# Kernel optimization log

Measured on AMD Instinct MI355X. Metric: run time of the kernel, lower is better.

Reference implementation:

```python
import jax, jax.numpy as jnp
import numpy as np

B, T, C, H, W = 16, 5, 512, 16, 16
NUM_FEAT = 10
K_IN = T * H * W          # 1280, conv1/G3 in_channels
G_OUT = NUM_FEAT * H * W  # 2560, G3 out_channels


def setup_inputs() -> dict:
    key = jax.random.key(0)
    ks = jax.random.split(key, 9)
    inp = {
        "input": jax.random.normal(ks[0], (B, T, C, H, W), dtype=jnp.float32),
        "input1": jax.random.normal(ks[1], (B, T, C, H, W), dtype=jnp.float32),
        "act_weights": jax.random.uniform(ks[2], (3,), dtype=jnp.float32),
        # Conv1d kernels with kernel_size=1 stored as [out_ch, in_ch]
        "conv1_w": jax.random.normal(ks[3], (NUM_FEAT, K_IN), dtype=jnp.float32) / np.sqrt(K_IN),
        "conv1_b": jax.random.normal(ks[4], (NUM_FEAT,), dtype=jnp.float32) * 0.01,
        "G3_w": jax.random.normal(ks[5], (G_OUT, K_IN), dtype=jnp.float32) / np.sqrt(K_IN),
        "G3_b": jax.random.normal(ks[6], (G_OUT,), dtype=jnp.float32) * 0.01,
        "ffnn1_w": jax.random.normal(ks[7], (C, C), dtype=jnp.float32) / np.sqrt(C),
        "ffnn1_b": jax.random.normal(ks[8], (C,), dtype=jnp.float32) * 0.01,
    }
    return inp


def reference(input, input1, act_weights, conv1_w, conv1_b, G3_w, G3_b, ffnn1_w, ffnn1_b):
    b, t, c, h, w = input.shape
    nf = conv1_w.shape[0]
    # [B,T,C,H,W] -> [B,C,T*H*W] -> transpose to [B, T*H*W, C] (conv1d channel axis = T*H*W)
    x = jnp.transpose(input, (0, 2, 1, 3, 4)).reshape(b, c, t * h * w)
    x = jnp.swapaxes(x, 1, 2)  # [B, K_IN, C]

    # conv1 (1x1 conv == GEMM over channel axis): [B, nf, C]
    c1 = jnp.einsum("fk,bkc->bfc", conv1_w, x) + conv1_b[None, :, None]
    # transpose -> [B, C, nf]; AvgPool1d(nf) -> mean over nf -> [B, C]
    pooled = jnp.mean(jnp.swapaxes(c1, 1, 2), axis=-1)
    # shared linear (same ffnn1 used in all three branches)
    pre = pooled @ ffnn1_w.T + ffnn1_b  # [B, C]

    # G3: [B, G_OUT, C] -> permute -> [B, C, G_OUT]
    g3 = jnp.einsum("gk,bkc->bgc", G3_w, x) + G3_b[None, :, None]
    g3 = jnp.swapaxes(g3, 1, 2)  # [B, C, G_OUT]

    # diag_embed(v) @ M == v[..., None] * M  -> fuse the three branches into one scale
    scale = (act_weights[0] * jax.nn.relu(pre)
             + act_weights[1] * jax.nn.sigmoid(pre)
             + act_weights[2] * jax.nn.softmax(pre, axis=1))  # [B, C]

    out = scale[:, :, None] * g3  # [B, C, nf*H*W]
    out = out.reshape(b, c, nf, h, w)
    return jnp.transpose(out, (0, 2, 1, 3, 4))  # [B, nf, C, H, W]
```

## Files before the change

kernel.cpp:

```cpp
#include <hip/hip_runtime.h>
#include <hip/hip_bf16.h>
#include <stdint.h>

#define B_   16
#define T_   5
#define C_   512
#define HW_  256
#define NF_  10
#define KIN_ 1280
#define GOUT_ 2560

typedef __attribute__((ext_vector_type(8))) short s16x8;
typedef __attribute__((ext_vector_type(4))) float f32x4;
typedef unsigned short u16;

__device__ __forceinline__ u16 f2bf(float x) {
    unsigned int u = __float_as_uint(x);
    return (u16)((u + 0x7FFFu + ((u >> 16) & 1u)) >> 16);
}

#define CASTW_N8  (GOUT_ * KIN_ / 8)
#define CASTW_BLKS (CASTW_N8 / 256)

__global__ __launch_bounds__(256) void k_init(const float* __restrict__ conv1_w,
                        const float* __restrict__ conv1_b,
                        float* __restrict__ wbar, float* __restrict__ bbar,
                        const float* __restrict__ g3w,
                        u16* __restrict__ wsA) {
    if (blockIdx.x < 5) {
        int k = blockIdx.x * 256 + threadIdx.x;
        float s = 0.f;
        #pragma unroll
        for (int f = 0; f < NF_; ++f) s += conv1_w[f * KIN_ + k];
        wbar[k] = s * (1.0f / NF_);
        if (blockIdx.x == 0 && threadIdx.x == 0) {
            float sb = 0.f;
            #pragma unroll
            for (int f = 0; f < NF_; ++f) sb += conv1_b[f];
            *bbar = sb * (1.0f / NF_);
        }
        return;
    }
    int i = (blockIdx.x - 5) * 256 + threadIdx.x;
    if (i < CASTW_N8) {
        const float4* s = reinterpret_cast<const float4*>(g3w) + (size_t)i * 2;
        float4 v0 = s[0], v1 = s[1];
        union { u16 h[8]; int4 v; } u;
        u.h[0] = f2bf(v0.x); u.h[1] = f2bf(v0.y); u.h[2] = f2bf(v0.z); u.h[3] = f2bf(v0.w);
        u.h[4] = f2bf(v1.x); u.h[5] = f2bf(v1.y); u.h[6] = f2bf(v1.z); u.h[7] = f2bf(v1.w);
        reinterpret_cast<int4*>(wsA)[i] = u.v;
    }
}

__global__ void k_wbar(const float* __restrict__ conv1_w,
                       const float* __restrict__ conv1_b,
                       float* __restrict__ wbar, float* __restrict__ bbar) {
    int k = blockIdx.x * blockDim.x + threadIdx.x;
    if (k < KIN_) {
        float s = 0.f;
        #pragma unroll
        for (int f = 0; f < NF_; ++f) s += conv1_w[f * KIN_ + k];
        wbar[k] = s * (1.0f / NF_);
    }
    if (blockIdx.x == 0 && threadIdx.x == 0) {
        float s = 0.f;
        #pragma unroll
        for (int f = 0; f < NF_; ++f) s += conv1_b[f];
        *bbar = s * (1.0f / NF_);
    }
}

#define FUSE_BLKS (B_ * C_)

__global__ __launch_bounds__(256) void k_prep(const float* __restrict__ in,
                         const float* __restrict__ wbar,
                         const float* __restrict__ bbar,
                         float* __restrict__ pooled,
                         u16* __restrict__ X) {
    int bc = blockIdx.x;
    int b = bc >> 9;
    int c = bc & 511;
    int tid = threadIdx.x;

    float s = 0.f;
    if (tid < 160) {
        int t   = tid >> 5;
        int hw0 = (tid & 31) * 8;
        size_t off = ((size_t)(b * T_ + t) * C_ + c) * HW_ + hw0;
        const float4* ip = reinterpret_cast<const float4*>(in + off);
        float4 v0 = ip[0], v1 = ip[1];
        const float4* wp = reinterpret_cast<const float4*>(wbar + t * HW_ + hw0);
        float4 w0 = wp[0], w1 = wp[1];
        s = v0.x * w0.x + v0.y * w0.y + v0.z * w0.z + v0.w * w0.w
          + v1.x * w1.x + v1.y * w1.y + v1.z * w1.z + v1.w * w1.w;
        union { u16 h[8]; int4 q; } u;
        u.h[0] = f2bf(v0.x); u.h[1] = f2bf(v0.y); u.h[2] = f2bf(v0.z); u.h[3] = f2bf(v0.w);
        u.h[4] = f2bf(v1.x); u.h[5] = f2bf(v1.y); u.h[6] = f2bf(v1.z); u.h[7] = f2bf(v1.w);
        reinterpret_cast<int4*>(X + off)[0] = u.q;
    }

    #pragma unroll
    for (int off = 32; off > 0; off >>= 1) s += __shfl_down(s, off, 64);
    __shared__ float red[4];
    int wid = tid >> 6, lane = tid & 63;
    if (lane == 0) red[wid] = s;
    __syncthreads();
    if (tid == 0) {
        float tot = red[0] + red[1] + red[2] + red[3];
        pooled[bc] = tot + *bbar;
    }
}

__global__ __launch_bounds__(256) void k_pooled(const float* __restrict__ in,
                         const float* __restrict__ wbar,
                         const float* __restrict__ bbar,
                         float* __restrict__ pooled) {
    int bc = blockIdx.x;
    int b = bc >> 9;
    int c = bc & 511;
    int hw = threadIdx.x;
    const float* base = in + ((size_t)(b * T_) * C_ + c) * HW_;
    float s = 0.f;
    #pragma unroll
    for (int t = 0; t < T_; ++t)
        s = fmaf(wbar[t * HW_ + hw], base[(size_t)t * C_ * HW_ + hw], s);
    #pragma unroll
    for (int off = 32; off > 0; off >>= 1) s += __shfl_down(s, off, 64);
    __shared__ float red[4];
    int wid = threadIdx.x >> 6, lane = threadIdx.x & 63;
    if (lane == 0) red[wid] = s;
    __syncthreads();
    if (threadIdx.x == 0) {
        float tot = red[0] + red[1] + red[2] + red[3];
        pooled[bc] = tot + *bbar;
    }
}

__global__ __launch_bounds__(256) void k_pre(const float* __restrict__ pooled,
                       const float* __restrict__ ffnn1_w,
                       const float* __restrict__ ffnn1_b,
                       float* __restrict__ pre) {
    int b   = blockIdx.x >> 4;
    int grp = blockIdx.x & 15;
    int wid = threadIdx.x >> 6, lane = threadIdx.x & 63;

    const float4* pp = reinterpret_cast<const float4*>(pooled + b * C_ + lane * 8);
    float4 pa = pp[0], pb = pp[1];

    #pragma unroll
    for (int rr = 0; rr < 8; ++rr) {
        int c = grp * 32 + wid * 8 + rr;
        const float4* wr = reinterpret_cast<const float4*>(ffnn1_w + (size_t)c * C_ + lane * 8);
        float4 wa = wr[0], wb2 = wr[1];
        float d = pa.x * wa.x + pa.y * wa.y + pa.z * wa.z + pa.w * wa.w
                + pb.x * wb2.x + pb.y * wb2.y + pb.z * wb2.z + pb.w * wb2.w;
        #pragma unroll
        for (int off = 32; off > 0; off >>= 1) d += __shfl_xor(d, off, 64);
        if (lane == 0) pre[b * C_ + c] = d + ffnn1_b[c];
    }
}

__global__ __launch_bounds__(512) void k_scale(const float* __restrict__ pooled,
                        const float* __restrict__ ffnn1_w,
                        const float* __restrict__ ffnn1_b,
                        const float* __restrict__ actw,
                        float* __restrict__ scale) {
    int b = blockIdx.x;
    int c = threadIdx.x;
    __shared__ float sp[C_];
    __shared__ float red[8];

    sp[c] = pooled[b * C_ + c];
    __syncthreads();

    float acc = ffnn1_b[c];
    const float* wr = ffnn1_w + (size_t)c * C_;
    #pragma unroll 8
    for (int j = 0; j < C_; ++j) acc = fmaf(wr[j], sp[j], acc);

    int wid = c >> 6, lane = c & 63;
    float m = acc;
    #pragma unroll
    for (int off = 32; off > 0; off >>= 1) m = fmaxf(m, __shfl_down(m, off, 64));
    if (lane == 0) red[wid] = m;
    __syncthreads();
    if (c == 0) {
        float mm = red[0];
        #pragma unroll
        for (int i = 1; i < 8; ++i) mm = fmaxf(mm, red[i]);
        red[0] = mm;
    }
    __syncthreads();
    m = red[0];
    __syncthreads();

    float e = __expf(acc - m);
    float s = e;
    #pragma unroll
    for (int off = 32; off > 0; off >>= 1) s += __shfl_down(s, off, 64);
    if (lane == 0) red[wid] = s;
    __syncthreads();
    if (c == 0) {
        float ss = 0.f;
        #pragma unroll
        for (int i = 0; i < 8; ++i) ss += red[i];
        red[0] = ss;
    }
    __syncthreads();
    s = red[0];

    float w0 = actw[0], w1 = actw[1], w2 = actw[2];
    float val = w0 * fmaxf(acc, 0.f)
              + w1 * (1.f / (1.f + __expf(-acc)))
              + w2 * (e / s);
    scale[b * C_ + c] = val;
}

#define BM 320
#define BN 256
#define BK 32
#define NKT (KIN_ / BK)
#define ABUF (BM * BK)
#define BBUF (BN * BK)
#define BUFU (ABUF + BBUF)

__device__ __forceinline__ void gload16(const void* g, void* l) {
    __builtin_amdgcn_global_load_lds(
        (const __attribute__((address_space(1))) void*)g,
        (__attribute__((address_space(3))) void*)l, 16, 0, 0);
}

__global__ __launch_bounds__(512, 1) void k_gemm_mfma(
    const u16* __restrict__ A,
    const u16* __restrict__ X,
    const float* __restrict__ g3b,
    const float* __restrict__ pre,
    const float* __restrict__ actw,
    float* __restrict__ out)
{
    __shared__ u16 lds[3 * BUFU];
    __shared__ float sS[BN];
    __shared__ float redm[8], reds[8];

    int orig = blockIdx.x;
    int xcd  = orig & 7;
    int idx  = orig >> 3;
    int nt   = xcd * 4 + (idx >> 3);
    int gt   = idx & 7;
    int g0   = gt * BM;
    int b    = nt >> 1;
    int c0   = (nt & 1) * BN;

    int tid = threadIdx.x;
    int lane = tid & 63, wid = tid >> 6;
    int wr = wid >> 2, wc = wid & 3;
    int lrow = lane & 15, lslot = lane >> 4;

    int offA0, offA1, offA2, offB0, offB1;
    {
        int q, r, p;
        q = tid;         r = q >> 2; p = q & 3; offA0 = r * KIN_ + (p ^ ((r >> 1) & 3)) * 8;
        q = 512 + tid;   r = q >> 2; p = q & 3; offA1 = r * KIN_ + (p ^ ((r >> 1) & 3)) * 8;
        q = 1024 + tid;  r = q >> 2; p = q & 3; offA2 = r * KIN_ + (p ^ ((r >> 1) & 3)) * 8;
        q = tid;         r = q >> 2; p = q & 3; offB0 = r * HW_  + (p ^ ((r >> 1) & 3)) * 8;
        q = 512 + tid;   r = q >> 2; p = q & 3; offB1 = r * HW_  + (p ^ ((r >> 1) & 3)) * 8;
    }
    int wb = wid * 512;

    const u16* Abase = A + (size_t)g0 * KIN_;
    #define XOFF(kt) ((((size_t)(b * T_ + ((kt) >> 3)) * C_) + c0) * HW_ + ((kt) & 7) * 32)

    #define STAGE_H1(D, sA, sX)                                              \
    {                                                                        \
        gload16((sA) + offA0, (D) + wb);                                     \
        gload16((sA) + offA1, (D) + 4096 + wb);                              \
        gload16((sX) + offB0, (D) + ABUF + wb);                              \
    }
    #define STAGE_H2(D, sA, sX)                                              \
    {                                                                        \
        if (tid < 256) gload16((sA) + offA2, (D) + 8192 + wb);               \
        gload16((sX) + offB1, (D) + ABUF + 4096 + wb);                       \
    }

    {
        float p0 = pre[b * C_ + tid];
        float aw0 = actw[0], aw1 = actw[1], aw2 = actw[2];
        float mx = p0;
        #pragma unroll
        for (int off = 32; off > 0; off >>= 1) mx = fmaxf(mx, __shfl_xor(mx, off, 64));
        if (lane == 0) redm[wid] = mx;
        __syncthreads();
        float m8 = redm[0];
        #pragma unroll
        for (int i = 1; i < 8; ++i) m8 = fmaxf(m8, redm[i]);
        float e0 = __expf(p0 - m8);
        float sm = e0;
        #pragma unroll
        for (int off = 32; off > 0; off >>= 1) sm += __shfl_xor(sm, off, 64);
        if (lane == 0) reds[wid] = sm;
        __syncthreads();
        float ssum = reds[0];
        #pragma unroll
        for (int i = 1; i < 8; ++i) ssum += reds[i];
        if ((tid >> 8) == (c0 >> 8))
            sS[tid & 255] = aw0 * fmaxf(p0, 0.f)
                          + aw1 * (1.f / (1.f + __expf(-p0)))
                          + aw2 * (e0 / ssum);
    }

    STAGE_H1(lds, Abase, X + XOFF(0));
    STAGE_H2(lds, Abase, X + XOFF(0));
    STAGE_H1(lds + BUFU, Abase + BK, X + XOFF(1));
    STAGE_H2(lds + BUFU, Abase + BK, X + XOFF(1));
    if (tid < 256) asm volatile("s_waitcnt vmcnt(5)" ::: "memory");
    else           asm volatile("s_waitcnt vmcnt(4)" ::: "memory");
    __builtin_amdgcn_s_barrier();

    f32x4 acc[10][4];
    #pragma unroll
    for (int mI = 0; mI < 10; ++mI)
        #pragma unroll
        for (int n = 0; n < 4; ++n) acc[mI][n] = (f32x4)0.f;

    int cur = 0;
    for (int t = 0; t < NKT; ++t) {
        const u16* Ac = lds + cur * BUFU;
        const u16* Bc = Ac + ABUF;
        bool pre2 = (t + 2) < NKT;
        int nx = cur + 2; if (nx >= 3) nx -= 3;
        u16* Dn = lds + nx * BUFU;
        const u16* sA = Abase + (size_t)(t + 2) * BK;
        const u16* sX = X + XOFF(pre2 ? (t + 2) : 0);

        s16x8 b0[4], a0[5];
        #pragma unroll
        for (int n = 0; n < 4; ++n) {
            int r = wc * 64 + n * 16 + lrow;
            int p = lslot ^ ((r >> 1) & 3);
            b0[n] = *reinterpret_cast<const s16x8*>(Bc + r * BK + p * 8);
        }
        #pragma unroll
        for (int mI = 0; mI < 5; ++mI) {
            int r = wr * 160 + mI * 16 + lrow;
            int p = lslot ^ ((r >> 1) & 3);
            a0[mI] = *reinterpret_cast<const s16x8*>(Ac + r * BK + p * 8);
        }
        if (pre2) STAGE_H1(Dn, sA, sX);
        __builtin_amdgcn_s_barrier();
        asm volatile("s_waitcnt lgkmcnt(0)" ::: "memory");
        __builtin_amdgcn_sched_barrier(0);
        __builtin_amdgcn_s_setprio(1);
        #pragma unroll
        for (int mI = 0; mI < 5; ++mI)
            #pragma unroll
            for (int n = 0; n < 4; ++n)
                acc[mI][n] = __builtin_amdgcn_mfma_f32_16x16x32_bf16(
                                a0[mI], b0[n], acc[mI][n], 0, 0, 0);
        __builtin_amdgcn_s_setprio(0);

        s16x8 a1[5];
        #pragma unroll
        for (int mI = 0; mI < 5; ++mI) {
            int r = wr * 160 + (mI + 5) * 16 + lrow;
            int p = lslot ^ ((r >> 1) & 3);
            a1[mI] = *reinterpret_cast<const s16x8*>(Ac + r * BK + p * 8);
        }
        if (pre2) STAGE_H2(Dn, sA, sX);
        __builtin_amdgcn_s_barrier();
        asm volatile("s_waitcnt lgkmcnt(0)" ::: "memory");
        __builtin_amdgcn_sched_barrier(0);
        __builtin_amdgcn_s_setprio(1);
        #pragma unroll
        for (int mI = 0; mI < 5; ++mI)
            #pragma unroll
            for (int n = 0; n < 4; ++n)
                acc[mI + 5][n] = __builtin_amdgcn_mfma_f32_16x16x32_bf16(
                                    a1[mI], b0[n], acc[mI + 5][n], 0, 0, 0);
        __builtin_amdgcn_s_setprio(0);

        if (pre2) {
            if (tid < 256) asm volatile("s_waitcnt vmcnt(5)" ::: "memory");
            else           asm volatile("s_waitcnt vmcnt(4)" ::: "memory");
        } else {
            asm volatile("s_waitcnt vmcnt(0)" ::: "memory");
        }
        __builtin_amdgcn_s_barrier();
        ++cur; if (cur >= 3) cur -= 3;
    }

    #pragma unroll
    for (int n = 0; n < 4; ++n) {
        int cl = wc * 64 + n * 16 + lrow;
        int c  = c0 + cl;
        float sc = sS[cl];
        #pragma unroll
        for (int mI = 0; mI < 10; ++mI) {
            int g  = g0 + wr * 160 + mI * 16 + lslot * 4;
            int f  = g >> 8;
            int hw = g & 255;
            float4 bias = *reinterpret_cast<const float4*>(g3b + g);
            f32x4 v = acc[mI][n];
            float4 o;
            o.x = sc * (v[0] + bias.x);
            o.y = sc * (v[1] + bias.y);
            o.z = sc * (v[2] + bias.z);
            o.w = sc * (v[3] + bias.w);
            *reinterpret_cast<float4*>(
                out + (((size_t)(b * NF_ + f) * C_ + c) * HW_ + hw)) = o;
        }
    }
    #undef XOFF
    #undef STAGE_H1
    #undef STAGE_H2
}

#define FBM 128
#define FBN 128
#define FBK 32
__global__ __launch_bounds__(256) void k_gemm_fp32(
    const float* __restrict__ in,
    const float* __restrict__ g3w,
    const float* __restrict__ g3b,
    const float* __restrict__ scale,
    float* __restrict__ out)
{
    int b  = blockIdx.y;
    int gt = blockIdx.x >> 2;
    int ct = blockIdx.x & 3;
    int g0 = gt * FBM, c0 = ct * FBN;
    int tid = threadIdx.x;
    int ty = tid & 15;
    int tx = tid >> 4;

    __shared__ float As[FBK][FBM + 4];
    __shared__ float Bs[FBK][FBN + 4];

    float acc[8][8];
    #pragma unroll
    for (int i = 0; i < 8; ++i)
        #pragma unroll
        for (int j = 0; j < 8; ++j) acc[i][j] = 0.f;

    for (int k0 = 0; k0 < KIN_; k0 += FBK) {
        int t   = k0 >> 8;
        int hw0 = k0 & 255;
        #pragma unroll
        for (int p = 0; p < 16; ++p) {
            int idx = tid + p * 256;
            int kk = idx & 31, gg = idx >> 5;
            As[kk][gg] = g3w[(size_t)(g0 + gg) * KIN_ + k0 + kk];
        }
        const float* bsrc = in + ((size_t)(b * T_ + t) * C_ + c0) * HW_ + hw0;
        #pragma unroll
        for (int p = 0; p < 16; ++p) {
            int idx = tid + p * 256;
            int kk = idx & 31, cc = idx >> 5;
            Bs[kk][cc] = bsrc[(size_t)cc * HW_ + kk];
        }
        __syncthreads();
        #pragma unroll
        for (int kk = 0; kk < FBK; ++kk) {
            float a[8], bb[8];
            #pragma unroll
            for (int i = 0; i < 8; ++i) a[i] = As[kk][ty * 8 + i];
            #pragma unroll
            for (int j = 0; j < 8; ++j) bb[j] = Bs[kk][tx * 8 + j];
            #pragma unroll
            for (int i = 0; i < 8; ++i)
                #pragma unroll
                for (int j = 0; j < 8; ++j)
                    acc[i][j] = fmaf(a[i], bb[j], acc[i][j]);
        }
        __syncthreads();
    }

    int gl = ty * 8;
    int g  = g0 + gl;
    int f  = g >> 8;
    int hw = g & 255;
    #pragma unroll
    for (int j = 0; j < 8; ++j) {
        int c = c0 + tx * 8 + j;
        float sc = scale[b * C_ + c];
        float* op = out + (((size_t)(b * NF_ + f) * C_ + c) * HW_ + hw);
        float4 v0, v1;
        v0.x = sc * (acc[0][j] + g3b[g + 0]);
        v0.y = sc * (acc[1][j] + g3b[g + 1]);
        v0.z = sc * (acc[2][j] + g3b[g + 2]);
        v0.w = sc * (acc[3][j] + g3b[g + 3]);
        v1.x = sc * (acc[4][j] + g3b[g + 4]);
        v1.y = sc * (acc[5][j] + g3b[g + 5]);
        v1.z = sc * (acc[6][j] + g3b[g + 6]);
        v1.w = sc * (acc[7][j] + g3b[g + 7]);
        reinterpret_cast<float4*>(op)[0] = v0;
        reinterpret_cast<float4*>(op)[1] = v1;
    }
}

extern "C" void kernel_launch(void* const* d_in, const int* in_sizes, int n_in,
                              void* d_out, int out_size, void* d_ws, size_t ws_size,
                              hipStream_t stream) {
    const float* input    = (const float*)d_in[0];
    const float* actw     = (const float*)d_in[2];
    const float* conv1_w  = (const float*)d_in[3];
    const float* conv1_b  = (const float*)d_in[4];
    const float* g3w      = (const float*)d_in[5];
    const float* g3b      = (const float*)d_in[6];
    const float* ffnn1_w  = (const float*)d_in[7];
    const float* ffnn1_b  = (const float*)d_in[8];
    float* out = (float*)d_out;

    float* ws     = (float*)d_ws;
    float* wbar   = ws;
    float* bbar   = ws + KIN_;
    float* pooled = ws + 1536;
    float* pre    = ws + 1536 + B_ * C_;
    u16* wsA = (u16*)(ws + 17920);
    u16* wsX = wsA + (size_t)GOUT_ * KIN_;
    const size_t need = 71680ull + (size_t)GOUT_ * KIN_ * 2 + (size_t)B_ * T_ * C_ * HW_ * 2;

    if (ws_size >= need) {
        k_init<<<dim3(5 + CASTW_BLKS), dim3(256), 0, stream>>>(
            conv1_w, conv1_b, wbar, bbar, g3w, wsA);
        k_prep<<<dim3(FUSE_BLKS), dim3(256), 0, stream>>>(
            input, wbar, bbar, pooled, wsX);
        k_pre<<<dim3(256), dim3(256), 0, stream>>>(pooled, ffnn1_w, ffnn1_b, pre);
        k_gemm_mfma<<<dim3(256), dim3(512), 0, stream>>>(
            wsA, wsX, g3b, pre, actw, out);
    } else {
        k_wbar<<<dim3((KIN_ + 255) / 256), dim3(256), 0, stream>>>(conv1_w, conv1_b, wbar, bbar);
        k_pooled<<<dim3(B_ * C_), dim3(256), 0, stream>>>(input, wbar, bbar, pooled);
        k_scale<<<dim3(B_), dim3(512), 0, stream>>>(pooled, ffnn1_w, ffnn1_b, actw, pre);
        k_gemm_fp32<<<dim3((GOUT_ / FBM) * (C_ / FBN), B_), dim3(256), 0, stream>>>(
            input, g3w, g3b, pre, out);
    }
}
```

Before: 88.20 us.

## Split MFMA loop into four phases and move activation scale to separate kernel

The GEMM main loop is split into four MFMA phases instead of two. Each phase loads only part of the B fragments and issues one global-to-LDS prefetch, so LDS reads and prefetches interleave more finely with MFMA work and fewer fragment registers are live at once. The softmax/relu/sigmoid scale computation moves out of the GEMM prologue into a small k_act kernel that writes to the workspace, and the GEMM epilogue reads the scale from global memory. This adds one kernel launch and more barriers per k-step in exchange for a lighter GEMM prologue and finer overlap.

```diff
diff --git a/kernel.cpp b/kernel.cpp
--- a/kernel.cpp
+++ b/kernel.cpp
@@ -160,6 +160,39 @@
     }
 }
 
+__global__ __launch_bounds__(512) void k_act(const float* __restrict__ pre,
+                       const float* __restrict__ actw,
+                       float* __restrict__ scale) {
+    int b = blockIdx.x;
+    int tid = threadIdx.x;
+    int wid = tid >> 6, lane = tid & 63;
+    __shared__ float redm[8], reds[8];
+
+    float p0 = pre[b * C_ + tid];
+    float mx = p0;
+    #pragma unroll
+    for (int off = 32; off > 0; off >>= 1) mx = fmaxf(mx, __shfl_xor(mx, off, 64));
+    if (lane == 0) redm[wid] = mx;
+    __syncthreads();
+    float m8 = redm[0];
+    #pragma unroll
+    for (int i = 1; i < 8; ++i) m8 = fmaxf(m8, redm[i]);
+    float e0 = __expf(p0 - m8);
+    float sm = e0;
+    #pragma unroll
+    for (int off = 32; off > 0; off >>= 1) sm += __shfl_xor(sm, off, 64);
+    if (lane == 0) reds[wid] = sm;
+    __syncthreads();
+    float ssum = reds[0];
+    #pragma unroll
+    for (int i = 1; i < 8; ++i) ssum += reds[i];
+
+    float aw0 = actw[0], aw1 = actw[1], aw2 = actw[2];
+    scale[b * C_ + tid] = aw0 * fmaxf(p0, 0.f)
+                        + aw1 * (1.f / (1.f + __expf(-p0)))
+                        + aw2 * (e0 / ssum);
+}
+
 __global__ __launch_bounds__(512) void k_scale(const float* __restrict__ pooled,
                         const float* __restrict__ ffnn1_w,
                         const float* __restrict__ ffnn1_b,
@@ -234,13 +267,10 @@
     const u16* __restrict__ A,
     const u16* __restrict__ X,
     const float* __restrict__ g3b,
-    const float* __restrict__ pre,
-    const float* __restrict__ actw,
+    const float* __restrict__ scale,
     float* __restrict__ out)
 {
     __shared__ u16 lds[3 * BUFU];
-    __shared__ float sS[BN];
-    __shared__ float redm[8], reds[8];
 
     int orig = blockIdx.x;
     int xcd  = orig & 7;
@@ -270,48 +300,17 @@
     const u16* Abase = A + (size_t)g0 * KIN_;
     #define XOFF(kt) ((((size_t)(b * T_ + ((kt) >> 3)) * C_) + c0) * HW_ + ((kt) & 7) * 32)
 
-    #define STAGE_H1(D, sA, sX)                                              \
+    #define STAGE_ALL(D, sA, sX)                                             \
     {                                                                        \
         gload16((sA) + offA0, (D) + wb);                                     \
         gload16((sA) + offA1, (D) + 4096 + wb);                              \
+        if (tid < 256) gload16((sA) + offA2, (D) + 8192 + wb);               \
         gload16((sX) + offB0, (D) + ABUF + wb);                              \
-    }
-    #define STAGE_H2(D, sA, sX)                                              \
-    {                                                                        \
-        if (tid < 256) gload16((sA) + offA2, (D) + 8192 + wb);               \
         gload16((sX) + offB1, (D) + ABUF + 4096 + wb);                       \
     }
 
-    {
-        float p0 = pre[b * C_ + tid];
-        float aw0 = actw[0], aw1 = actw[1], aw2 = actw[2];
-        float mx = p0;
-        #pragma unroll
-        for (int off = 32; off > 0; off >>= 1) mx = fmaxf(mx, __shfl_xor(mx, off, 64));
-        if (lane == 0) redm[wid] = mx;
-        __syncthreads();
-        float m8 = redm[0];
-        #pragma unroll
-        for (int i = 1; i < 8; ++i) m8 = fmaxf(m8, redm[i]);
-        float e0 = __expf(p0 - m8);
-        float sm = e0;
-        #pragma unroll
-        for (int off = 32; off > 0; off >>= 1) sm += __shfl_xor(sm, off, 64);
-        if (lane == 0) reds[wid] = sm;
-        __syncthreads();
-        float ssum = reds[0];
-        #pragma unroll
-        for (int i = 1; i < 8; ++i) ssum += reds[i];
-        if ((tid >> 8) == (c0 >> 8))
-            sS[tid & 255] = aw0 * fmaxf(p0, 0.f)
-                          + aw1 * (1.f / (1.f + __expf(-p0)))
-                          + aw2 * (e0 / ssum);
-    }
-
-    STAGE_H1(lds, Abase, X + XOFF(0));
-    STAGE_H2(lds, Abase, X + XOFF(0));
-    STAGE_H1(lds + BUFU, Abase + BK, X + XOFF(1));
-    STAGE_H2(lds + BUFU, Abase + BK, X + XOFF(1));
+    STAGE_ALL(lds,        Abase,      X + XOFF(0));
+    STAGE_ALL(lds + BUFU, Abase + BK, X + XOFF(1));
     if (tid < 256) asm volatile("s_waitcnt vmcnt(5)" ::: "memory");
     else           asm volatile("s_waitcnt vmcnt(4)" ::: "memory");
     __builtin_amdgcn_s_barrier();
@@ -332,52 +331,72 @@
         const u16* sA = Abase + (size_t)(t + 2) * BK;
         const u16* sX = X + XOFF(pre2 ? (t + 2) : 0);
 
-        s16x8 b0[4], a0[5];
-        #pragma unroll
-        for (int n = 0; n < 4; ++n) {
-            int r = wc * 64 + n * 16 + lrow;
-            int p = lslot ^ ((r >> 1) & 3);
-            b0[n] = *reinterpret_cast<const s16x8*>(Bc + r * BK + p * 8);
-        }
-        #pragma unroll
-        for (int mI = 0; mI < 5; ++mI) {
-            int r = wr * 160 + mI * 16 + lrow;
-            int p = lslot ^ ((r >> 1) & 3);
-            a0[mI] = *reinterpret_cast<const s16x8*>(Ac + r * BK + p * 8);
-        }
-        if (pre2) STAGE_H1(Dn, sA, sX);
+        s16x8 b0, b1, b2, b3, a0[5], a1[5];
+
+        {
+            int r0 = wc * 64 + lrow,     p0 = lslot ^ ((r0 >> 1) & 3);
+            int r1 = wc * 64 + 16 + lrow, p1 = lslot ^ ((r1 >> 1) & 3);
+            b0 = *reinterpret_cast<const s16x8*>(Bc + r0 * BK + p0 * 8);
+            b1 = *reinterpret_cast<const s16x8*>(Bc + r1 * BK + p1 * 8);
+            #pragma unroll
+            for (int mI = 0; mI < 5; ++mI) {
+                int r = wr * 160 + mI * 16 + lrow;
+                int p = lslot ^ ((r >> 1) & 3);
+                a0[mI] = *reinterpret_cast<const s16x8*>(Ac + r * BK + p * 8);
+            }
+        }
+        if (pre2) gload16(sA + offA0, Dn + wb);
         __builtin_amdgcn_s_barrier();
         asm volatile("s_waitcnt lgkmcnt(0)" ::: "memory");
         __builtin_amdgcn_sched_barrier(0);
         __builtin_amdgcn_s_setprio(1);
         #pragma unroll
-        for (int mI = 0; mI < 5; ++mI)
-            #pragma unroll
-            for (int n = 0; n < 4; ++n)
-                acc[mI][n] = __builtin_amdgcn_mfma_f32_16x16x32_bf16(
-                                a0[mI], b0[n], acc[mI][n], 0, 0, 0);
+        for (int mI = 0; mI < 5; ++mI) {
+            acc[mI][0] = __builtin_amdgcn_mfma_f32_16x16x32_bf16(a0[mI], b0, acc[mI][0], 0, 0, 0);
+            acc[mI][1] = __builtin_amdgcn_mfma_f32_16x16x32_bf16(a0[mI], b1, acc[mI][1], 0, 0, 0);
+        }
         __builtin_amdgcn_s_setprio(0);
 
-        s16x8 a1[5];
+        {
+            int r2 = wc * 64 + 32 + lrow, p2 = lslot ^ ((r2 >> 1) & 3);
+            int r3 = wc * 64 + 48 + lrow, p3 = lslot ^ ((r3 >> 1) & 3);
+            b2 = *reinterpret_cast<const s16x8*>(Bc + r2 * BK + p2 * 8);
+            b3 = *reinterpret_cast<const s16x8*>(Bc + r3 * BK + p3 * 8);
+        }
+        if (pre2) gload16(sA + offA1, Dn + 4096 + wb);
+        __builtin_amdgcn_s_barrier();
+        asm volatile("s_waitcnt lgkmcnt(0)" ::: "memory");
+        __builtin_amdgcn_sched_barrier(0);
+        __builtin_amdgcn_s_setprio(1);
+        #pragma unroll
+        for (int mI = 0; mI < 5; ++mI) {
+            acc[mI][2] = __builtin_amdgcn_mfma_f32_16x16x32_bf16(a0[mI], b2, acc[mI][2], 0, 0, 0);
+            acc[mI][3] = __builtin_amdgcn_mfma_f32_16x16x32_bf16(a0[mI], b3, acc[mI][3], 0, 0, 0);
+        }
+        __builtin_amdgcn_s_setprio(0);
+
         #pragma unroll
         for (int mI = 0; mI < 5; ++mI) {
             int r = wr * 160 + (mI + 5) * 16 + lrow;
             int p = lslot ^ ((r >> 1) & 3);
             a1[mI] = *reinterpret_cast<const s16x8*>(Ac + r * BK + p * 8);
         }
-        if (pre2) STAGE_H2(Dn, sA, sX);
+        if (pre2) {
+            if (tid < 256) gload16(sA + offA2, Dn + 8192 + wb);
+            gload16(sX + offB0, Dn + ABUF + wb);
+        }
         __builtin_amdgcn_s_barrier();
         asm volatile("s_waitcnt lgkmcnt(0)" ::: "memory");
         __builtin_amdgcn_sched_barrier(0);
         __builtin_amdgcn_s_setprio(1);
         #pragma unroll
-        for (int mI = 0; mI < 5; ++mI)
-            #pragma unroll
-            for (int n = 0; n < 4; ++n)
-                acc[mI + 5][n] = __builtin_amdgcn_mfma_f32_16x16x32_bf16(
-                                    a1[mI], b0[n], acc[mI + 5][n], 0, 0, 0);
+        for (int mI = 0; mI < 5; ++mI) {
+            acc[mI + 5][0] = __builtin_amdgcn_mfma_f32_16x16x32_bf16(a1[mI], b0, acc[mI + 5][0], 0, 0, 0);
+            acc[mI + 5][1] = __builtin_amdgcn_mfma_f32_16x16x32_bf16(a1[mI], b1, acc[mI + 5][1], 0, 0, 0);
+        }
         __builtin_amdgcn_s_setprio(0);
 
+        if (pre2) gload16(sX + offB1, Dn + ABUF + 4096 + wb);
         if (pre2) {
             if (tid < 256) asm volatile("s_waitcnt vmcnt(5)" ::: "memory");
             else           asm volatile("s_waitcnt vmcnt(4)" ::: "memory");
@@ -385,14 +404,21 @@
             asm volatile("s_waitcnt vmcnt(0)" ::: "memory");
         }
         __builtin_amdgcn_s_barrier();
+        __builtin_amdgcn_s_setprio(1);
+        #pragma unroll
+        for (int mI = 0; mI < 5; ++mI) {
+            acc[mI + 5][2] = __builtin_amdgcn_mfma_f32_16x16x32_bf16(a1[mI], b2, acc[mI + 5][2], 0, 0, 0);
+            acc[mI + 5][3] = __builtin_amdgcn_mfma_f32_16x16x32_bf16(a1[mI], b3, acc[mI + 5][3], 0, 0, 0);
+        }
+        __builtin_amdgcn_s_setprio(0);
+
         ++cur; if (cur >= 3) cur -= 3;
     }
 
     #pragma unroll
     for (int n = 0; n < 4; ++n) {
-        int cl = wc * 64 + n * 16 + lrow;
-        int c  = c0 + cl;
-        float sc = sS[cl];
+        int c = c0 + wc * 64 + n * 16 + lrow;
+        float sc = scale[b * C_ + c];
         #pragma unroll
         for (int mI = 0; mI < 10; ++mI) {
             int g  = g0 + wr * 160 + mI * 16 + lslot * 4;
@@ -410,8 +436,7 @@
         }
     }
     #undef XOFF
-    #undef STAGE_H1
-    #undef STAGE_H2
+    #undef STAGE_ALL
 }
 
 #define FBM 128
@@ -515,6 +540,7 @@
     float* bbar   = ws + KIN_;
     float* pooled = ws + 1536;
     float* pre    = ws + 1536 + B_ * C_;
+    float* scale  = pooled;
     u16* wsA = (u16*)(ws + 17920);
     u16* wsX = wsA + (size_t)GOUT_ * KIN_;
     const size_t need = 71680ull + (size_t)GOUT_ * KIN_ * 2 + (size_t)B_ * T_ * C_ * HW_ * 2;
@@ -525,8 +551,9 @@
         k_prep<<<dim3(FUSE_BLKS), dim3(256), 0, stream>>>(
             input, wbar, bbar, pooled, wsX);
         k_pre<<<dim3(256), dim3(256), 0, stream>>>(pooled, ffnn1_w, ffnn1_b, pre);
+        k_act<<<dim3(B_), dim3(512), 0, stream>>>(pre, actw, scale);
         k_gemm_mfma<<<dim3(256), dim3(512), 0, stream>>>(
-            wsA, wsX, g3b, pre, actw, out);
+            wsA, wsX, g3b, scale, out);
     } else {
         k_wbar<<<dim3((KIN_ + 255) / 256), dim3(256), 0, stream>>>(conv1_w, conv1_b, wbar, bbar);
         k_pooled<<<dim3(B_ * C_), dim3(256), 0, stream>>>(input, wbar, bbar, pooled);
```

Result: faster. 86.19 us (-2.3%).
